# Performance work log

Hardware: AMD Instinct MI355X
Metric: run time of the kernel (lower is better)

## Reference

```python
import jax, jax.numpy as jnp
import numpy as np

RES = 512
RANK = 48
OUT = 32
N = 1_000_000
INIT = 0.1


def _contract_linf(xyz, aabb):
    # L-infinity cuboid contraction of unbounded coords into [-1,1]^3.
    center = (aabb[:3] + aabb[3:]) * 0.5
    half = jnp.maximum((aabb[3:] - aabb[:3]) * 0.5, 1e-6)
    x = (xyz - center) / half
    linf = jnp.max(jnp.abs(x), axis=-1, keepdims=True)
    safe = jnp.maximum(linf, 1.0)
    scale = jnp.where(linf > 1.0, (2.0 - 1.0 / safe) / safe, 1.0)
    return jnp.clip(x * scale, -1.0, 1.0)


def _sample_plane(plane, gx, gy):
    # plane: [R, Res, Res]; gx,gy in [-1,1] shape [N]; bilinear, align_corners=True.
    res = plane.shape[-1]
    fx = (gx + 1.0) * 0.5 * (res - 1)
    fy = (gy + 1.0) * 0.5 * (res - 1)
    x0 = jnp.clip(jnp.floor(fx), 0, res - 2).astype(jnp.int32)
    y0 = jnp.clip(jnp.floor(fy), 0, res - 2).astype(jnp.int32)
    wx = fx - x0
    wy = fy - y0
    x1 = x0 + 1
    y1 = y0 + 1
    # gathers -> [R, N]
    v = (plane[:, y0, x0] * ((1 - wy) * (1 - wx))
         + plane[:, y0, x1] * ((1 - wy) * wx)
         + plane[:, y1, x0] * (wy * (1 - wx))
         + plane[:, y1, x1] * (wy * wx))
    return v


def _sample_line(line, g):
    # line: [R, Res]; 1-D linear interp along the resolution axis (align_corners=True).
    res = line.shape[-1]
    f = (g + 1.0) * 0.5 * (res - 1)
    i0 = jnp.clip(jnp.floor(f), 0, res - 2).astype(jnp.int32)
    w = f - i0
    return line[:, i0] * (1 - w) + line[:, i0 + 1] * w  # [R, N]


def setup_inputs() -> dict:
    key = jax.random.key(0)
    ks = jax.random.split(key, 9)
    coordinates = jax.random.normal(ks[0], (N, 3), dtype=jnp.float32) * 1.5  # some points outside aabb
    aabb = jnp.array([-1.0, -1.0, -1.0, 1.0, 1.0, 1.0], dtype=jnp.float32)
    plane_xy = jax.random.normal(ks[1], (RANK, RES, RES), dtype=jnp.float32) * INIT
    plane_xz = jax.random.normal(ks[2], (RANK, RES, RES), dtype=jnp.float32) * INIT
    plane_yz = jax.random.normal(ks[3], (RANK, RES, RES), dtype=jnp.float32) * INIT
    line_z = jax.random.normal(ks[4], (RANK, RES), dtype=jnp.float32) * INIT
    line_y = jax.random.normal(ks[5], (RANK, RES), dtype=jnp.float32) * INIT
    line_x = jax.random.normal(ks[6], (RANK, RES), dtype=jnp.float32) * INIT
    W = jax.random.normal(ks[7], (OUT, RANK), dtype=jnp.float32) * INIT
    b = jnp.zeros((OUT,), dtype=jnp.float32)
    return {"coordinates": coordinates, "aabb": aabb,
            "plane_xy": plane_xy, "plane_xz": plane_xz, "plane_yz": plane_yz,
            "line_z": line_z, "line_y": line_y, "line_x": line_x,
            "W": W, "b": b}


def reference(coordinates, aabb, plane_xy, plane_xz, plane_yz, line_z, line_y, line_x, W, b):
    c = _contract_linf(coordinates, aabb)  # [N,3] in [-1,1]
    cx, cy, cz = c[:, 0], c[:, 1], c[:, 2]
    # VM decomposition: plane(a,b) * line(c), summed over the three permutations -> [R, N]
    vm = (_sample_plane(plane_xy, cx, cy) * _sample_line(line_z, cz)
          + _sample_plane(plane_xz, cx, cz) * _sample_line(line_y, cy)
          + _sample_plane(plane_yz, cy, cz) * _sample_line(line_x, cx))
    # projection rank -> out_channels: [N, OUT]
    return jnp.einsum('rn,or->no', vm, W) + b
```

## Files before the change

### kernel.cpp

```cpp
#include <hip/hip_runtime.h>
#include <stdint.h>

#define RES 512
#define RANK 48
#define OUT_CH 32
#define KBITS 5
#define NBKT (1 << (3 * KBITS))
#define STR 24

typedef unsigned int u32;
typedef unsigned short u16;
typedef u32 u32x4 __attribute__((ext_vector_type(4)));


static __device__ __forceinline__ u16 f2bf(float f){
  u32 u = __float_as_uint(f);
  u32 r = (u + 0x7fffu + ((u >> 16) & 1u)) >> 16;
  return (u16)r;
}

static __device__ __forceinline__ void axis_setup(float c, int& o, float& w){
  float f = (c + 1.f) * 255.5f;
  float of = fminf(fmaxf(floorf(f), 0.f), 510.f);
  o = (int)of; w = f - of;
}

static __device__ __forceinline__ void contract(const float* __restrict__ aabb,
                                                float px, float py, float pz,
                                                float& cx, float& cy, float& cz){
  float c0 = (aabb[0] + aabb[3]) * 0.5f;
  float c1 = (aabb[1] + aabb[4]) * 0.5f;
  float c2 = (aabb[2] + aabb[5]) * 0.5f;
  float h0 = fmaxf((aabb[3] - aabb[0]) * 0.5f, 1e-6f);
  float h1 = fmaxf((aabb[4] - aabb[1]) * 0.5f, 1e-6f);
  float h2 = fmaxf((aabb[5] - aabb[2]) * 0.5f, 1e-6f);
  float x0 = (px - c0) / h0;
  float x1 = (py - c1) / h1;
  float x2 = (pz - c2) / h2;
  float linf = fmaxf(fabsf(x0), fmaxf(fabsf(x1), fabsf(x2)));
  float scale = 1.f;
  if (linf > 1.f){ float inv = 1.f / linf; scale = (2.f - inv) * inv; }
  cx = fminf(fmaxf(x0 * scale, -1.f), 1.f);
  cy = fminf(fmaxf(x1 * scale, -1.f), 1.f);
  cz = fminf(fmaxf(x2 * scale, -1.f), 1.f);
}

static __device__ __forceinline__ u32 spread3(u32 x){
  x &= 0x3FF;
  x = (x | (x << 16)) & 0x030000FF;
  x = (x | (x <<  8)) & 0x0300F00F;
  x = (x | (x <<  4)) & 0x030C30C3;
  x = (x | (x <<  2)) & 0x09249249;
  return x;
}

static __device__ __forceinline__ u32 morton_key(float cx, float cy, float cz){
  u32 kx = (u32)fminf(fmaxf((cx + 1.f) * 16.f, 0.f), 31.f);
  u32 ky = (u32)fminf(fmaxf((cy + 1.f) * 16.f, 0.f), 31.f);
  u32 kz = (u32)fminf(fmaxf((cz + 1.f) * 16.f, 0.f), 31.f);
  return spread3(kx) | (spread3(ky) << 1) | (spread3(kz) << 2);
}


__global__ void zero_hist(u32* __restrict__ hist)
{
  hist[blockIdx.x * 1024 + threadIdx.x] = 0u;
}


#define TRANS_P 3072
#define TRANS_L 6

__global__ void prep_fused(const float* __restrict__ pxy, const float* __restrict__ pxz,
                           const float* __restrict__ pyz,
                           const float* __restrict__ lz, const float* __restrict__ ly,
                           const float* __restrict__ lx,
                           const float* __restrict__ coords, const float* __restrict__ aabb,
                           u32* __restrict__ dstP, u32* __restrict__ dstL,
                           u32* __restrict__ hist, u32* __restrict__ keyrank, int n)
{
  __shared__ u32 lds[256 * 25];
  int bid = blockIdx.x;
  int tid = threadIdx.x;
  if (bid < TRANS_P){
    int xh = bid & 1, y = (bid >> 1) & 511, p = bid >> 10;
    const float* src = (p == 0) ? pxy : (p == 1) ? pxz : pyz;
    int x = xh * 256 + tid;
    #pragma unroll
    for (int r2 = 0; r2 < 24; ++r2){
      float f0 = src[((size_t)(2 * r2) * RES + y) * RES + x];
      float f1 = src[((size_t)(2 * r2 + 1) * RES + y) * RES + x];
      lds[tid * 25 + r2] = (u32)f2bf(f0) | ((u32)f2bf(f1) << 16);
    }
    __syncthreads();
    u32* dplane = dstP + (size_t)p * (RES * RES * STR);
    size_t base = ((size_t)y * RES + xh * 256) * STR;
    for (int t = tid; t < 256 * STR; t += 256){
      dplane[base + t] = lds[t + t / 24];
    }
  } else if (bid < TRANS_P + TRANS_L){
    int g = (bid - TRANS_P) * 256 + tid;
    if (g < 3 * RES){
      int p = g >> 9, i = g & 511;
      const float* src = (p == 0) ? lz : (p == 1) ? ly : lx;
      u32* d = dstL + (size_t)g * STR;
      #pragma unroll
      for (int r2 = 0; r2 < 24; ++r2){
        float f0 = src[(2 * r2) * RES + i];
        float f1 = src[(2 * r2 + 1) * RES + i];
        d[r2] = (u32)f2bf(f0) | ((u32)f2bf(f1) << 16);
      }
    }
  } else {
    int i = (bid - TRANS_P - TRANS_L) * 256 + tid;
    if (i < n){
      float cx, cy, cz;
      contract(aabb, coords[3*i], coords[3*i+1], coords[3*i+2], cx, cy, cz);
      u32 key = morton_key(cx, cy, cz);
      u32 rank = atomicAdd(hist + key, 1u);
      keyrank[i] = (rank << 15) | key;
    }
  }
}


__global__ void scan_kernel(u32* __restrict__ hist)
{
  __shared__ u32 part[1024];
  int tid = threadIdx.x;
  int base = tid * 32;
  u32 loc[32];
  u32 s = 0;
  #pragma unroll
  for (int j = 0; j < 32; j++){ loc[j] = hist[base + j]; s += loc[j]; }
  part[tid] = s;
  __syncthreads();
  for (int off = 1; off < 1024; off <<= 1){
    u32 v = 0;
    if (tid >= off) v = part[tid - off];
    __syncthreads();
    part[tid] += v;
    __syncthreads();
  }
  u32 run = part[tid] - s;
  #pragma unroll
  for (int j = 0; j < 32; j++){ u32 t = loc[j]; hist[base + j] = run; run += t; }
}


__global__ void key_scatter(const float* __restrict__ coords, const float* __restrict__ aabb,
                            const u32* __restrict__ base, const u32* __restrict__ keyrank,
                            float4* __restrict__ sorted, int n)
{
  int i = blockIdx.x * 256 + threadIdx.x;
  if (i >= n) return;
  float cx, cy, cz;
  contract(aabb, coords[3*i], coords[3*i+1], coords[3*i+2], cx, cy, cz);
  u32 kr = keyrank[i];
  u32 pos = base[kr & 0x7FFFu] + (kr >> 15);
  sorted[pos] = make_float4(cx, cy, cz, __uint_as_float((u32)i));
}


#define EXLO(u) __uint_as_float((u) << 16)
#define EXHI(u) __uint_as_float((u) & 0xffff0000u)

static __device__ __forceinline__ void build_lv(float lv[RANK], const u32* __restrict__ p, float w){
  #pragma unroll
  for (int j = 0; j < 6; j++){
    u32x4 a = *(const u32x4*)(p + 4 * j);
    u32x4 b = *(const u32x4*)(p + STR + 4 * j);
    #pragma unroll
    for (int k = 0; k < 4; k++){
      int r = (j * 4 + k) * 2;
      float lo0 = EXLO(a[k]), hi0 = EXHI(a[k]);
      float lo1 = EXLO(b[k]), hi1 = EXHI(b[k]);
      lv[r]     = fmaf(w, lo1 - lo0, lo0);
      lv[r + 1] = fmaf(w, hi1 - hi0, hi0);
    }
  }
}

static __device__ __forceinline__ void acc_corner(float vm[RANK], const float lv[RANK],
                                                  const u32* __restrict__ p, float wc){
  #pragma unroll
  for (int j = 0; j < 6; j++){
    u32x4 t = *(const u32x4*)(p + 4 * j);
    #pragma unroll
    for (int k = 0; k < 4; k++){
      int r = (j * 4 + k) * 2;
      vm[r]     = fmaf(EXLO(t[k]) * lv[r],     wc, vm[r]);
      vm[r + 1] = fmaf(EXHI(t[k]) * lv[r + 1], wc, vm[r + 1]);
    }
  }
}

static __device__ __forceinline__ void geo_core(int ox, int oy, int oz,
    float wx, float wy, float wz,
    const u32* __restrict__ pl, const u32* __restrict__ ln,
    const float* __restrict__ Wt, const float* __restrict__ bias,
    float* __restrict__ acc)
{
  float uxw = 1.f - wx, uyw = 1.f - wy, uzw = 1.f - wz;

  const u32* A  = pl + ((size_t)oy * RES + ox) * STR;
  const u32* B  = pl + (size_t)RES * RES * STR     + ((size_t)oz * RES + ox) * STR;
  const u32* C  = pl + (size_t)2 * RES * RES * STR + ((size_t)oz * RES + oy) * STR;
  const u32* LZp = ln +                          (size_t)oz * STR;
  const u32* LYp = ln + (size_t)RES * STR     + (size_t)oy * STR;
  const u32* LXp = ln + (size_t)2 * RES * STR + (size_t)ox * STR;

  float vm[RANK];
  #pragma unroll
  for (int r = 0; r < RANK; r++) vm[r] = 0.f;

  float lv[RANK];

  build_lv(lv, LZp, wz);
  acc_corner(vm, lv, A,                  uyw * uxw);
  acc_corner(vm, lv, A + STR,            uyw * wx);
  acc_corner(vm, lv, A + RES * STR,      wy * uxw);
  acc_corner(vm, lv, A + RES * STR + STR, wy * wx);

  build_lv(lv, LYp, wy);
  acc_corner(vm, lv, B,                  uzw * uxw);
  acc_corner(vm, lv, B + STR,            uzw * wx);
  acc_corner(vm, lv, B + RES * STR,      wz * uxw);
  acc_corner(vm, lv, B + RES * STR + STR, wz * wx);

  build_lv(lv, LXp, wx);
  acc_corner(vm, lv, C,                  uzw * uyw);
  acc_corner(vm, lv, C + STR,            uzw * wy);
  acc_corner(vm, lv, C + RES * STR,      wz * uyw);
  acc_corner(vm, lv, C + RES * STR + STR, wz * wy);

  #pragma unroll
  for (int o = 0; o < 8; o++){
    float4 bv = *(const float4*)(bias + o * 4);
    acc[4*o+0] = bv.x; acc[4*o+1] = bv.y; acc[4*o+2] = bv.z; acc[4*o+3] = bv.w;
  }
  const float4* Wt4 = (const float4*)Wt;
  #pragma unroll
  for (int r = 0; r < RANK; r++){
    float v = vm[r];
    const float4* wrow = Wt4 + r * 8;
    #pragma unroll
    for (int q = 0; q < 8; q++){
      float4 w4 = wrow[q];
      acc[4*q+0] = fmaf(v, w4.x, acc[4*q+0]); acc[4*q+1] = fmaf(v, w4.y, acc[4*q+1]);
      acc[4*q+2] = fmaf(v, w4.z, acc[4*q+2]); acc[4*q+3] = fmaf(v, w4.w, acc[4*q+3]);
    }
  }
}


__global__ __launch_bounds__(256, 2)
void geo_sorted(const float4* __restrict__ sorted,
                const u32* __restrict__ pl, const u32* __restrict__ ln,
                const float* __restrict__ W, const float* __restrict__ bias,
                float* __restrict__ out, int n, int nwg)
{
  __shared__ __align__(16) float Wt[RANK * OUT_CH];
  for (int t = threadIdx.x; t < RANK * OUT_CH; t += 256){
    int r = t >> 5, o = t & 31;
    Wt[t] = W[o * RANK + r];
  }
  __syncthreads();

  int bid = blockIdx.x;
  int q = nwg >> 3, r8 = nwg & 7;
  int xcd = bid & 7, sub = bid >> 3;
  int swz = (xcd < r8 ? xcd * (q + 1) : r8 * (q + 1) + (xcd - r8) * q) + sub;

  int i = swz * 256 + threadIdx.x;
  if (i >= n) return;

  u32x4 pr = __builtin_nontemporal_load((const u32x4*)(sorted + i));
  float cx = __uint_as_float(pr[0]);
  float cy = __uint_as_float(pr[1]);
  float cz = __uint_as_float(pr[2]);
  u32 oidx = pr[3];

  int ox, oy, oz; float wx, wy, wz;
  axis_setup(cx, ox, wx); axis_setup(cy, oy, wy); axis_setup(cz, oz, wz);

  float acc[OUT_CH];
  geo_core(ox, oy, oz, wx, wy, wz, pl, ln, Wt, bias, acc);

  float4* o4 = (float4*)(out + (size_t)oidx * 32);
  #pragma unroll
  for (int qq = 0; qq < 8; qq++)
    o4[qq] = make_float4(acc[4*qq+0], acc[4*qq+1], acc[4*qq+2], acc[4*qq+3]);
}


__global__ __launch_bounds__(256, 2)
void geo_unsorted(const float* __restrict__ coords, const float* __restrict__ aabb,
                  const u32* __restrict__ pl, const u32* __restrict__ ln,
                  const float* __restrict__ W, const float* __restrict__ bias,
                  float* __restrict__ out, int n)
{
  __shared__ __align__(16) float Wt[RANK * OUT_CH];
  for (int t = threadIdx.x; t < RANK * OUT_CH; t += 256){
    int r = t >> 5, o = t & 31;
    Wt[t] = W[o * RANK + r];
  }
  __syncthreads();

  int i = blockIdx.x * 256 + threadIdx.x;
  if (i >= n) return;

  float cx, cy, cz;
  contract(aabb, coords[3*i], coords[3*i+1], coords[3*i+2], cx, cy, cz);
  int ox, oy, oz; float wx, wy, wz;
  axis_setup(cx, ox, wx); axis_setup(cy, oy, wy); axis_setup(cz, oz, wz);

  float acc[OUT_CH];
  geo_core(ox, oy, oz, wx, wy, wz, pl, ln, Wt, bias, acc);

  float4* o4 = (float4*)(out + (size_t)i * 32);
  #pragma unroll
  for (int qq = 0; qq < 8; qq++)
    o4[qq] = make_float4(acc[4*qq+0], acc[4*qq+1], acc[4*qq+2], acc[4*qq+3]);
}


__global__ __launch_bounds__(256, 2)
void geo_direct(const float* __restrict__ coords, const float* __restrict__ aabb,
                const float* __restrict__ PXY, const float* __restrict__ PXZ, const float* __restrict__ PYZ,
                const float* __restrict__ LZ, const float* __restrict__ LY, const float* __restrict__ LX,
                const float* __restrict__ W, const float* __restrict__ bias,
                float* __restrict__ out, int n)
{
  __shared__ __align__(16) float Wt[RANK * OUT_CH];
  for (int t = threadIdx.x; t < RANK * OUT_CH; t += 256){
    int r = t >> 5, o = t & 31;
    Wt[t] = W[o * RANK + r];
  }
  __syncthreads();

  int i = blockIdx.x * 256 + threadIdx.x;
  if (i >= n) return;

  float cx, cy, cz;
  contract(aabb, coords[3*i], coords[3*i+1], coords[3*i+2], cx, cy, cz);
  int ox, oy, oz; float wx, wy, wz;
  axis_setup(cx, ox, wx); axis_setup(cy, oy, wy); axis_setup(cz, oz, wz);

  int offA = oy * RES + ox, offB = oz * RES + ox, offC = oz * RES + oy;
  float uxw = 1.f - wx, uyw = 1.f - wy, uzw = 1.f - wz;
  float aw00 = uyw*uxw, aw01 = uyw*wx, aw10 = wy*uxw, aw11 = wy*wx;
  float bw00 = uzw*uxw, bw01 = uzw*wx, bw10 = wz*uxw, bw11 = wz*wx;
  float cw00 = uzw*uyw, cw01 = uzw*wy, cw10 = wz*uyw, cw11 = wz*wy;

  float acc[OUT_CH];
  #pragma unroll
  for (int o = 0; o < 8; o++){
    float4 bv = *(const float4*)(bias + o * 4);
    acc[4*o+0] = bv.x; acc[4*o+1] = bv.y; acc[4*o+2] = bv.z; acc[4*o+3] = bv.w;
  }
  const float4* Wt4 = (const float4*)Wt;

  for (int r = 0; r < RANK; r++){
    const float* pA = PXY + (size_t)r * RES * RES;
    const float* pB = PXZ + (size_t)r * RES * RES;
    const float* pC = PYZ + (size_t)r * RES * RES;
    float va = fmaf(pA[offA], aw00, fmaf(pA[offA+1], aw01, fmaf(pA[offA+RES], aw10, pA[offA+RES+1]*aw11)));
    float vb = fmaf(pB[offB], bw00, fmaf(pB[offB+1], bw01, fmaf(pB[offB+RES], bw10, pB[offB+RES+1]*bw11)));
    float vc = fmaf(pC[offC], cw00, fmaf(pC[offC+1], cw01, fmaf(pC[offC+RES], cw10, pC[offC+RES+1]*cw11)));
    float l0;
    l0 = LZ[r * RES + oz];
    float lzv = fmaf(wz, LZ[r * RES + oz + 1] - l0, l0);
    l0 = LY[r * RES + oy];
    float lyv = fmaf(wy, LY[r * RES + oy + 1] - l0, l0);
    l0 = LX[r * RES + ox];
    float lxv = fmaf(wx, LX[r * RES + ox + 1] - l0, l0);
    float vm = fmaf(va, lzv, fmaf(vb, lyv, vc * lxv));
    const float4* wrow = Wt4 + r * 8;
    #pragma unroll
    for (int q = 0; q < 8; q++){
      float4 w4 = wrow[q];
      acc[4*q+0] = fmaf(vm, w4.x, acc[4*q+0]); acc[4*q+1] = fmaf(vm, w4.y, acc[4*q+1]);
      acc[4*q+2] = fmaf(vm, w4.z, acc[4*q+2]); acc[4*q+3] = fmaf(vm, w4.w, acc[4*q+3]);
    }
  }

  float4* o4 = (float4*)(out + (size_t)i * 32);
  #pragma unroll
  for (int q = 0; q < 8; q++)
    o4[q] = make_float4(acc[4*q+0], acc[4*q+1], acc[4*q+2], acc[4*q+3]);
}


extern "C" void kernel_launch(void* const* d_in, const int* in_sizes, int n_in,
                              void* d_out, int out_size, void* d_ws, size_t ws_size,
                              hipStream_t stream)
{
  const float* coords = (const float*)d_in[0];
  const float* aabb   = (const float*)d_in[1];
  const float* pxy    = (const float*)d_in[2];
  const float* pxz    = (const float*)d_in[3];
  const float* pyz    = (const float*)d_in[4];
  const float* lz     = (const float*)d_in[5];
  const float* ly     = (const float*)d_in[6];
  const float* lx     = (const float*)d_in[7];
  const float* W      = (const float*)d_in[8];
  const float* bias   = (const float*)d_in[9];
  float* out = (float*)d_out;
  int n = in_sizes[0] / 3;
  int nwg = (n + 255) / 256;

  const size_t planesU = (size_t)3 * RES * RES * STR;
  const size_t linesU  = (size_t)3 * RES * STR;
  const size_t histU   = NBKT;
  const size_t keyrU   = (size_t)n;
  const size_t sortedU = (size_t)4 * n;
  const size_t needFull = (planesU + linesU + histU + keyrU + sortedU) * 4;

  if (ws_size >= needFull){
    u32* pl      = (u32*)d_ws;
    u32* ln      = pl + planesU;
    u32* hist    = ln + linesU;
    u32* keyrank = hist + histU;
    float4* sorted = (float4*)(keyrank + keyrU);
    zero_hist<<<NBKT / 1024, 1024, 0, stream>>>(hist);
    prep_fused<<<TRANS_P + TRANS_L + nwg, 256, 0, stream>>>(
        pxy, pxz, pyz, lz, ly, lx, coords, aabb, pl, ln, hist, keyrank, n);
    scan_kernel<<<1, 1024, 0, stream>>>(hist);
    key_scatter<<<nwg, 256, 0, stream>>>(coords, aabb, hist, keyrank, sorted, n);
    geo_sorted<<<nwg, 256, 0, stream>>>(sorted, pl, ln, W, bias, out, n, nwg);
  } else if (ws_size >= (planesU + linesU) * 4){
    u32* pl = (u32*)d_ws;
    u32* ln = pl + planesU;
    prep_fused<<<TRANS_P + TRANS_L, 256, 0, stream>>>(
        pxy, pxz, pyz, lz, ly, lx, coords, aabb, pl, ln, (u32*)pl, (u32*)pl, 0);
    geo_unsorted<<<nwg, 256, 0, stream>>>(coords, aabb, pl, ln, W, bias, out, n);
  } else {
    geo_direct<<<nwg, 256, 0, stream>>>(coords, aabb, pxy, pxz, pyz, lz, ly, lx, W, bias, out, n);
  }
}
```

Baseline: 365.4 us.

## Split each point across 8 cooperating threads with padded 32-word texel rows

The texel stride is padded from 24 to 32 words so each of 8 lanes owns a 16-byte slice of the 48 bf16 ranks. The gather kernel now assigns 8 threads per point, each sampling its 8 ranks, then exchanges partial rank vectors through LDS so each thread computes 4 output channels. This removes the heavy per-thread register footprint (48-rank vm plus 32 accumulators) and makes each texel fetch a coalesced 128-byte read across 8 lanes. In exchange the plane buffer grows by a third, and the kernel adds a shared-memory round trip, a block barrier and 8x as many blocks.

After: 339.2 us. -7.2%, faster.

```diff
diff --git a/kernel.cpp b/kernel.cpp
--- a/kernel.cpp
+++ b/kernel.cpp
@@ -6,7 +6,7 @@
 #define OUT_CH 32
 #define KBITS 5
 #define NBKT (1 << (3 * KBITS))
-#define STR 24
+#define STR 32
 
 typedef unsigned int u32;
 typedef unsigned short u16;
@@ -96,7 +96,8 @@
     u32* dplane = dstP + (size_t)p * (RES * RES * STR);
     size_t base = ((size_t)y * RES + xh * 256) * STR;
     for (int t = tid; t < 256 * STR; t += 256){
-      dplane[base + t] = lds[t + t / 24];
+      int tex = t >> 5, r = t & 31;
+      dplane[base + t] = (r < 24) ? lds[tex * 25 + r] : 0u;
     }
   } else if (bid < TRANS_P + TRANS_L){
     int g = (bid - TRANS_P) * 256 + tid;
@@ -110,6 +111,8 @@
         float f1 = src[(2 * r2 + 1) * RES + i];
         d[r2] = (u32)f2bf(f0) | ((u32)f2bf(f1) << 16);
       }
+      #pragma unroll
+      for (int r2 = 24; r2 < STR; ++r2) d[r2] = 0u;
     }
   } else {
     int i = (bid - TRANS_P - TRANS_L) * 256 + tid;
@@ -165,163 +168,157 @@
 #define EXLO(u) __uint_as_float((u) << 16)
 #define EXHI(u) __uint_as_float((u) & 0xffff0000u)
 
-static __device__ __forceinline__ void build_lv(float lv[RANK], const u32* __restrict__ p, float w){
-  #pragma unroll
-  for (int j = 0; j < 6; j++){
-    u32x4 a = *(const u32x4*)(p + 4 * j);
-    u32x4 b = *(const u32x4*)(p + STR + 4 * j);
-    #pragma unroll
-    for (int k = 0; k < 4; k++){
-      int r = (j * 4 + k) * 2;
-      float lo0 = EXLO(a[k]), hi0 = EXHI(a[k]);
-      float lo1 = EXLO(b[k]), hi1 = EXHI(b[k]);
-      lv[r]     = fmaf(w, lo1 - lo0, lo0);
-      lv[r + 1] = fmaf(w, hi1 - hi0, hi0);
-    }
-  }
-}
-
-static __device__ __forceinline__ void acc_corner(float vm[RANK], const float lv[RANK],
-                                                  const u32* __restrict__ p, float wc){
-  #pragma unroll
-  for (int j = 0; j < 6; j++){
-    u32x4 t = *(const u32x4*)(p + 4 * j);
-    #pragma unroll
-    for (int k = 0; k < 4; k++){
-      int r = (j * 4 + k) * 2;
-      vm[r]     = fmaf(EXLO(t[k]) * lv[r],     wc, vm[r]);
-      vm[r + 1] = fmaf(EXHI(t[k]) * lv[r + 1], wc, vm[r + 1]);
-    }
-  }
-}
-
-static __device__ __forceinline__ void geo_core(int ox, int oy, int oz,
-    float wx, float wy, float wz,
-    const u32* __restrict__ pl, const u32* __restrict__ ln,
-    const float* __restrict__ Wt, const float* __restrict__ bias,
-    float* __restrict__ acc)
-{
-  float uxw = 1.f - wx, uyw = 1.f - wy, uzw = 1.f - wz;
-
-  const u32* A  = pl + ((size_t)oy * RES + ox) * STR;
-  const u32* B  = pl + (size_t)RES * RES * STR     + ((size_t)oz * RES + ox) * STR;
-  const u32* C  = pl + (size_t)2 * RES * RES * STR + ((size_t)oz * RES + oy) * STR;
-  const u32* LZp = ln +                          (size_t)oz * STR;
-  const u32* LYp = ln + (size_t)RES * STR     + (size_t)oy * STR;
-  const u32* LXp = ln + (size_t)2 * RES * STR + (size_t)ox * STR;
-
-  float vm[RANK];
-  #pragma unroll
-  for (int r = 0; r < RANK; r++) vm[r] = 0.f;
-
-  float lv[RANK];
-
-  build_lv(lv, LZp, wz);
-  acc_corner(vm, lv, A,                  uyw * uxw);
-  acc_corner(vm, lv, A + STR,            uyw * wx);
-  acc_corner(vm, lv, A + RES * STR,      wy * uxw);
-  acc_corner(vm, lv, A + RES * STR + STR, wy * wx);
-
-  build_lv(lv, LYp, wy);
-  acc_corner(vm, lv, B,                  uzw * uxw);
-  acc_corner(vm, lv, B + STR,            uzw * wx);
-  acc_corner(vm, lv, B + RES * STR,      wz * uxw);
-  acc_corner(vm, lv, B + RES * STR + STR, wz * wx);
-
-  build_lv(lv, LXp, wx);
-  acc_corner(vm, lv, C,                  uzw * uyw);
-  acc_corner(vm, lv, C + STR,            uzw * wy);
-  acc_corner(vm, lv, C + RES * STR,      wz * uyw);
-  acc_corner(vm, lv, C + RES * STR + STR, wz * wy);
-
-  #pragma unroll
-  for (int o = 0; o < 8; o++){
-    float4 bv = *(const float4*)(bias + o * 4);
-    acc[4*o+0] = bv.x; acc[4*o+1] = bv.y; acc[4*o+2] = bv.z; acc[4*o+3] = bv.w;
-  }
-  const float4* Wt4 = (const float4*)Wt;
-  #pragma unroll
-  for (int r = 0; r < RANK; r++){
-    float v = vm[r];
-    const float4* wrow = Wt4 + r * 8;
-    #pragma unroll
-    for (int q = 0; q < 8; q++){
-      float4 w4 = wrow[q];
-      acc[4*q+0] = fmaf(v, w4.x, acc[4*q+0]); acc[4*q+1] = fmaf(v, w4.y, acc[4*q+1]);
-      acc[4*q+2] = fmaf(v, w4.z, acc[4*q+2]); acc[4*q+3] = fmaf(v, w4.w, acc[4*q+3]);
-    }
-  }
-}
-
-
+#define CORN_INIT(ps, taddr, wc) \
+  { u32x4 _t = *(const u32x4*)(taddr); \
+    _Pragma("unroll") for (int c = 0; c < 4; c++){ \
+      ps[2*c] = EXLO(_t[c]) * (wc); ps[2*c+1] = EXHI(_t[c]) * (wc); } }
+
+#define CORN_ACC(ps, taddr, wc) \
+  { u32x4 _t = *(const u32x4*)(taddr); \
+    _Pragma("unroll") for (int c = 0; c < 4; c++){ \
+      ps[2*c] = fmaf(EXLO(_t[c]), (wc), ps[2*c]); ps[2*c+1] = fmaf(EXHI(_t[c]), (wc), ps[2*c+1]); } }
+
+template<bool SORTED>
 __global__ __launch_bounds__(256, 2)
-void geo_sorted(const float4* __restrict__ sorted,
-                const u32* __restrict__ pl, const u32* __restrict__ ln,
-                const float* __restrict__ W, const float* __restrict__ bias,
-                float* __restrict__ out, int n, int nwg)
-{
-  __shared__ __align__(16) float Wt[RANK * OUT_CH];
-  for (int t = threadIdx.x; t < RANK * OUT_CH; t += 256){
-    int r = t >> 5, o = t & 31;
-    Wt[t] = W[o * RANK + r];
+void geo_coop(const float4* __restrict__ sorted,
+              const float* __restrict__ coords, const float* __restrict__ aabb,
+              const u32* __restrict__ pl, const u32* __restrict__ ln,
+              const float* __restrict__ W, const float* __restrict__ bias,
+              float* __restrict__ out, int n, int nwg)
+{
+  __shared__ __align__(16) float Wlds[8 * 49 * 4];
+  __shared__ __align__(16) float vmlds[32][68];
+
+  for (int e = threadIdx.x; e < 8 * RANK * 4; e += 256){
+    int k = e / (RANK * 4);
+    int rem = e - k * (RANK * 4);
+    int r = rem >> 2, j = rem & 3;
+    Wlds[(k * 49 + r) * 4 + j] = W[(4 * k + j) * RANK + r];
   }
   __syncthreads();
 
   int bid = blockIdx.x;
-  int q = nwg >> 3, r8 = nwg & 7;
-  int xcd = bid & 7, sub = bid >> 3;
-  int swz = (xcd < r8 ? xcd * (q + 1) : r8 * (q + 1) + (xcd - r8) * q) + sub;
-
-  int i = swz * 256 + threadIdx.x;
-  if (i >= n) return;
-
-  u32x4 pr = __builtin_nontemporal_load((const u32x4*)(sorted + i));
-  float cx = __uint_as_float(pr[0]);
-  float cy = __uint_as_float(pr[1]);
-  float cz = __uint_as_float(pr[2]);
-  u32 oidx = pr[3];
+  int swz;
+  if (SORTED){
+    int q = nwg >> 3, r8 = nwg & 7;
+    int xcd = bid & 7, sub = bid >> 3;
+    swz = (xcd < r8 ? xcd * (q + 1) : r8 * (q + 1) + (xcd - r8) * q) + sub;
+  } else {
+    swz = bid;
+  }
+
+  int g = threadIdx.x >> 3;
+  int k = threadIdx.x & 7;
+  int i = swz * 32 + g;
+  bool valid = i < n;
+  int ic = valid ? i : (n - 1);
+
+  float cx, cy, cz; u32 oidx;
+  if (SORTED){
+    u32x4 pr = __builtin_nontemporal_load((const u32x4*)(sorted + ic));
+    cx = __uint_as_float(pr[0]);
+    cy = __uint_as_float(pr[1]);
+    cz = __uint_as_float(pr[2]);
+    oidx = pr[3];
+  } else {
+    contract(aabb, coords[3*ic], coords[3*ic+1], coords[3*ic+2], cx, cy, cz);
+    oidx = (u32)ic;
+  }
 
   int ox, oy, oz; float wx, wy, wz;
   axis_setup(cx, ox, wx); axis_setup(cy, oy, wy); axis_setup(cz, oz, wz);
-
-  float acc[OUT_CH];
-  geo_core(ox, oy, oz, wx, wy, wz, pl, ln, Wt, bias, acc);
-
-  float4* o4 = (float4*)(out + (size_t)oidx * 32);
-  #pragma unroll
-  for (int qq = 0; qq < 8; qq++)
-    o4[qq] = make_float4(acc[4*qq+0], acc[4*qq+1], acc[4*qq+2], acc[4*qq+3]);
-}
-
-
-__global__ __launch_bounds__(256, 2)
-void geo_unsorted(const float* __restrict__ coords, const float* __restrict__ aabb,
-                  const u32* __restrict__ pl, const u32* __restrict__ ln,
-                  const float* __restrict__ W, const float* __restrict__ bias,
-                  float* __restrict__ out, int n)
-{
-  __shared__ __align__(16) float Wt[RANK * OUT_CH];
-  for (int t = threadIdx.x; t < RANK * OUT_CH; t += 256){
-    int r = t >> 5, o = t & 31;
-    Wt[t] = W[o * RANK + r];
-  }
+  float uxw = 1.f - wx, uyw = 1.f - wy, uzw = 1.f - wz;
+
+  const u32* A   = pl + ((size_t)oy * RES + ox) * STR + 4 * k;
+  const u32* B   = pl + (size_t)RES * RES * STR     + ((size_t)oz * RES + ox) * STR + 4 * k;
+  const u32* C   = pl + (size_t)2 * RES * RES * STR + ((size_t)oz * RES + oy) * STR + 4 * k;
+  const u32* LZp = ln +                          (size_t)oz * STR + 4 * k;
+  const u32* LYp = ln + (size_t)RES * STR     + (size_t)oy * STR + 4 * k;
+  const u32* LXp = ln + (size_t)2 * RES * STR + (size_t)ox * STR + 4 * k;
+
+  float vm8[8];
+  #pragma unroll
+  for (int j = 0; j < 8; j++) vm8[j] = 0.f;
+
+  {
+    u32x4 l0 = *(const u32x4*)(LZp);
+    u32x4 l1 = *(const u32x4*)(LZp + STR);
+    float lv8[8], ps8[8];
+    #pragma unroll
+    for (int c = 0; c < 4; c++){
+      float a0 = EXLO(l0[c]), a1 = EXHI(l0[c]);
+      float b0 = EXLO(l1[c]), b1 = EXHI(l1[c]);
+      lv8[2*c]   = fmaf(wz, b0 - a0, a0);
+      lv8[2*c+1] = fmaf(wz, b1 - a1, a1);
+    }
+    CORN_INIT(ps8, A,                 uyw * uxw);
+    CORN_ACC (ps8, A + STR,           uyw * wx);
+    CORN_ACC (ps8, A + RES * STR,     wy * uxw);
+    CORN_ACC (ps8, A + RES * STR + STR, wy * wx);
+    #pragma unroll
+    for (int j = 0; j < 8; j++) vm8[j] = fmaf(ps8[j], lv8[j], vm8[j]);
+  }
+  {
+    u32x4 l0 = *(const u32x4*)(LYp);
+    u32x4 l1 = *(const u32x4*)(LYp + STR);
+    float lv8[8], ps8[8];
+    #pragma unroll
+    for (int c = 0; c < 4; c++){
+      float a0 = EXLO(l0[c]), a1 = EXHI(l0[c]);
+      float b0 = EXLO(l1[c]), b1 = EXHI(l1[c]);
+      lv8[2*c]   = fmaf(wy, b0 - a0, a0);
+      lv8[2*c+1] = fmaf(wy, b1 - a1, a1);
+    }
+    CORN_INIT(ps8, B,                 uzw * uxw);
+    CORN_ACC (ps8, B + STR,           uzw * wx);
+    CORN_ACC (ps8, B + RES * STR,     wz * uxw);
+    CORN_ACC (ps8, B + RES * STR + STR, wz * wx);
+    #pragma unroll
+    for (int j = 0; j < 8; j++) vm8[j] = fmaf(ps8[j], lv8[j], vm8[j]);
+  }
+  {
+    u32x4 l0 = *(const u32x4*)(LXp);
+    u32x4 l1 = *(const u32x4*)(LXp + STR);
+    float lv8[8], ps8[8];
+    #pragma unroll
+    for (int c = 0; c < 4; c++){
+      float a0 = EXLO(l0[c]), a1 = EXHI(l0[c]);
+      float b0 = EXLO(l1[c]), b1 = EXHI(l1[c]);
+      lv8[2*c]   = fmaf(wx, b0 - a0, a0);
+      lv8[2*c+1] = fmaf(wx, b1 - a1, a1);
+    }
+    CORN_INIT(ps8, C,                 uzw * uyw);
+    CORN_ACC (ps8, C + STR,           uzw * wy);
+    CORN_ACC (ps8, C + RES * STR,     wz * uyw);
+    CORN_ACC (ps8, C + RES * STR + STR, wz * wy);
+    #pragma unroll
+    for (int j = 0; j < 8; j++) vm8[j] = fmaf(ps8[j], lv8[j], vm8[j]);
+  }
+
+  *(float4*)&vmlds[g][8 * k]     = make_float4(vm8[0], vm8[1], vm8[2], vm8[3]);
+  *(float4*)&vmlds[g][8 * k + 4] = make_float4(vm8[4], vm8[5], vm8[6], vm8[7]);
   __syncthreads();
 
-  int i = blockIdx.x * 256 + threadIdx.x;
-  if (i >= n) return;
-
-  float cx, cy, cz;
-  contract(aabb, coords[3*i], coords[3*i+1], coords[3*i+2], cx, cy, cz);
-  int ox, oy, oz; float wx, wy, wz;
-  axis_setup(cx, ox, wx); axis_setup(cy, oy, wy); axis_setup(cz, oz, wz);
-
-  float acc[OUT_CH];
-  geo_core(ox, oy, oz, wx, wy, wz, pl, ln, Wt, bias, acc);
-
-  float4* o4 = (float4*)(out + (size_t)i * 32);
-  #pragma unroll
-  for (int qq = 0; qq < 8; qq++)
-    o4[qq] = make_float4(acc[4*qq+0], acc[4*qq+1], acc[4*qq+2], acc[4*qq+3]);
+  float vmv[RANK];
+  #pragma unroll
+  for (int qd = 0; qd < 12; qd++){
+    float4 v4 = *(const float4*)&vmlds[g][qd * 4];
+    vmv[4*qd+0] = v4.x; vmv[4*qd+1] = v4.y; vmv[4*qd+2] = v4.z; vmv[4*qd+3] = v4.w;
+  }
+  float4 accv = ((const float4*)bias)[k];
+  const float4* wk = (const float4*)(Wlds + (size_t)k * 49 * 4);
+  #pragma unroll
+  for (int r = 0; r < RANK; r++){
+    float4 w4 = wk[r];
+    accv.x = fmaf(vmv[r], w4.x, accv.x);
+    accv.y = fmaf(vmv[r], w4.y, accv.y);
+    accv.z = fmaf(vmv[r], w4.z, accv.z);
+    accv.w = fmaf(vmv[r], w4.w, accv.w);
+  }
+
+  if (valid){
+    *(float4*)(out + (size_t)oidx * 32 + 4 * k) = accv;
+  }
 }
 
 
@@ -408,7 +405,8 @@
   const float* bias   = (const float*)d_in[9];
   float* out = (float*)d_out;
   int n = in_sizes[0] / 3;
-  int nwg = (n + 255) / 256;
+  int nwg256 = (n + 255) / 256;
+  int nwg32  = (n + 31) / 32;
 
   const size_t planesU = (size_t)3 * RES * RES * STR;
   const size_t linesU  = (size_t)3 * RES * STR;
@@ -424,18 +422,18 @@
     u32* keyrank = hist + histU;
     float4* sorted = (float4*)(keyrank + keyrU);
     zero_hist<<<NBKT / 1024, 1024, 0, stream>>>(hist);
-    prep_fused<<<TRANS_P + TRANS_L + nwg, 256, 0, stream>>>(
+    prep_fused<<<TRANS_P + TRANS_L + nwg256, 256, 0, stream>>>(
         pxy, pxz, pyz, lz, ly, lx, coords, aabb, pl, ln, hist, keyrank, n);
     scan_kernel<<<1, 1024, 0, stream>>>(hist);
-    key_scatter<<<nwg, 256, 0, stream>>>(coords, aabb, hist, keyrank, sorted, n);
-    geo_sorted<<<nwg, 256, 0, stream>>>(sorted, pl, ln, W, bias, out, n, nwg);
+    key_scatter<<<nwg256, 256, 0, stream>>>(coords, aabb, hist, keyrank, sorted, n);
+    geo_coop<true><<<nwg32, 256, 0, stream>>>(sorted, nullptr, nullptr, pl, ln, W, bias, out, n, nwg32);
   } else if (ws_size >= (planesU + linesU) * 4){
     u32* pl = (u32*)d_ws;
     u32* ln = pl + planesU;
     prep_fused<<<TRANS_P + TRANS_L, 256, 0, stream>>>(
         pxy, pxz, pyz, lz, ly, lx, coords, aabb, pl, ln, (u32*)pl, (u32*)pl, 0);
-    geo_unsorted<<<nwg, 256, 0, stream>>>(coords, aabb, pl, ln, W, bias, out, n);
+    geo_coop<false><<<nwg32, 256, 0, stream>>>(nullptr, coords, aabb, pl, ln, W, bias, out, n, nwg32);
   } else {
-    geo_direct<<<nwg, 256, 0, stream>>>(coords, aabb, pxy, pxz, pyz, lz, ly, lx, W, bias, out, n);
-  }
-}
+    geo_direct<<<nwg256, 256, 0, stream>>>(coords, aabb, pxy, pxz, pyz, lz, ly, lx, W, bias, out, n);
+  }
+}
```
